# Kernel optimization log

Measured on AMD Instinct MI355X. Metric: run time of the kernel, lower is better.

## Reference

```python
import jax, jax.numpy as jnp
import numpy as np

NEG_INF = jnp.float32(-9e15)
LEAKY_SLOPE = jnp.float32(0.01)  # torch nn.LeakyReLU default


def setup_inputs() -> dict:
    key = jax.random.key(0)
    k1, k2, k3, k4, k5 = jax.random.split(key, 5)
    B, N, din, draw, T = 128, 10000, 64, 64, 8
    D = din + draw
    x = jax.random.normal(k1, (B, N, din), dtype=jnp.float32)
    raw_x = jax.random.normal(k2, (B, N, draw), dtype=jnp.float32)
    # xavier_uniform with gain=1.414 over (D, 1) fan dims
    bound = 1.414 * float(np.sqrt(6.0 / (D + 1)))
    a = jax.random.uniform(k3, (T, D, 1), dtype=jnp.float32, minval=-bound, maxval=bound)
    adj_mask = jax.random.randint(k4, (N,), 0, 2).astype(jnp.float32)
    type_index = jax.random.randint(k5, (B,), 0, T)
    return {"x": x, "raw_x": raw_x, "a": a, "adj_mask": adj_mask,
            "node_index": 0, "type_index": type_index}


def reference(x, raw_x, a, adj_mask, node_index, type_index):
    B, N, _ = x.shape
    T = a.shape[0]
    # broadcast target node features to all nodes and concat with raw features
    target = x[:, node_index, :]                                   # [B, din]
    concat = jnp.concatenate(
        [jnp.broadcast_to(target[:, None, :], (B, N, target.shape[-1])), raw_x],
        axis=-1)                                                   # [B, N, D]
    # per-type additive attention logits (tiny projection D -> 1 per type)
    e = jnp.einsum('bnd,tdo->btn', concat, a)                      # [B, T, N]
    e = jnp.where(e > 0, e, LEAKY_SLOPE * e)                       # LeakyReLU
    masked = jnp.where(adj_mask[None, None, :] > 0, e, NEG_INF)
    att = jax.nn.softmax(masked, axis=-1) * adj_mask[None, None, :]  # [B, T, N]
    # select the attention row matching each sample's type via one-hot
    onehot = jax.nn.one_hot(type_index, T, dtype=att.dtype)        # [B, T]
    probs = jnp.einsum('btn,bt->bn', att, onehot)                  # [B, N]
    return probs
```

## Files before the change

### kernel.cpp

```cpp
#include <hip/hip_runtime.h>
#include <math.h>

#define NEG_INF_F (-9000000000000000.0f)
#define SLOPE 0.01f

constexpr int B_ = 128, N_ = 10000, DIN = 64, DRAW = 64;
constexpr int CHUNK = 1024;
constexpr int NCHUNK = (N_ + CHUNK - 1) / CHUNK;

__global__ __launch_bounds__(256) void pass1_kernel(
    const float* __restrict__ x, const float* __restrict__ raw_x,
    const float* __restrict__ a, const float* __restrict__ adj,
    const int* __restrict__ node_index, const int* __restrict__ type_index,
    float* __restrict__ e_buf, float* __restrict__ pm, float* __restrict__ ps)
{
    const int b = blockIdx.y;
    const int c = blockIdx.x;
    const int tid = threadIdx.x;
    const int t = type_index[b];

    __shared__ float a2[64];
    __shared__ float s_cb;

    if (tid < 64) {
        a2[tid] = a[t * 128 + 64 + tid];
        const int ni = node_index[0];
        float v = x[((size_t)b * N_ + ni) * DIN + tid] * a[t * 128 + tid];
        for (int off = 32; off > 0; off >>= 1) v += __shfl_down(v, off);
        if (tid == 0) s_cb = v;
    }
    __syncthreads();
    const float cb = s_cb;

    float m = NEG_INF_F;
    float s = 0.f;

    const int n0 = c * CHUNK;
    const int n1 = (n0 + CHUNK < N_) ? (n0 + CHUNK) : N_;
    for (int n = n0 + tid; n < n1; n += 256) {
        if (adj[n] > 0.f) {
            const float4* row = (const float4*)(raw_x + ((size_t)b * N_ + n) * DRAW);
            float acc = 0.f;
#pragma unroll
            for (int k = 0; k < 16; ++k) {
                float4 r = row[k];
                acc += r.x * a2[4 * k + 0] + r.y * a2[4 * k + 1]
                     + r.z * a2[4 * k + 2] + r.w * a2[4 * k + 3];
            }
            float e = cb + acc;
            e = (e > 0.f) ? e : SLOPE * e;
            e_buf[(size_t)b * N_ + n] = e;
            if (e > m) { s = s * __expf(m - e) + 1.f; m = e; }
            else       { s += __expf(e - m); }
        }
    }

    __shared__ float sm[256];
    __shared__ float ss[256];
    sm[tid] = m; ss[tid] = s;
    __syncthreads();
    for (int off = 128; off > 0; off >>= 1) {
        if (tid < off) {
            float m2 = sm[tid + off], s2 = ss[tid + off];
            float M = fmaxf(sm[tid], m2);
            ss[tid] = ss[tid] * __expf(sm[tid] - M) + s2 * __expf(m2 - M);
            sm[tid] = M;
        }
        __syncthreads();
    }
    if (tid == 0) {
        pm[b * NCHUNK + c] = sm[0];
        ps[b * NCHUNK + c] = ss[0];
    }
}

__global__ __launch_bounds__(64) void merge_kernel(
    const float* __restrict__ pm, const float* __restrict__ ps,
    float* __restrict__ Mb, float* __restrict__ invSb)
{
    const int b = blockIdx.x;
    const int tid = threadIdx.x;
    float m = NEG_INF_F, s = 0.f;
    if (tid < NCHUNK) { m = pm[b * NCHUNK + tid]; s = ps[b * NCHUNK + tid]; }
    for (int off = 32; off > 0; off >>= 1) {
        float m2 = __shfl_down(m, off);
        float s2 = __shfl_down(s, off);
        float M = fmaxf(m, m2);
        s = s * __expf(m - M) + s2 * __expf(m2 - M);
        m = M;
    }
    if (tid == 0) { Mb[b] = m; invSb[b] = 1.f / s; }
}

__global__ __launch_bounds__(256) void pass3_kernel(
    const float* __restrict__ e_buf, const float* __restrict__ adj,
    const float* __restrict__ Mb, const float* __restrict__ invSb,
    float* __restrict__ out)
{
    const int b = blockIdx.y;
    const int n = blockIdx.x * 256 + threadIdx.x;
    if (n >= N_) return;
    const size_t i = (size_t)b * N_ + n;
    float o = 0.f;
    if (adj[n] > 0.f) o = __expf(e_buf[i] - Mb[b]) * invSb[b];
    out[i] = o;
}

extern "C" void kernel_launch(void* const* d_in, const int* in_sizes, int n_in,
                              void* d_out, int out_size, void* d_ws, size_t ws_size,
                              hipStream_t stream) {
    const float* x     = (const float*)d_in[0];
    const float* raw_x = (const float*)d_in[1];
    const float* a     = (const float*)d_in[2];
    const float* adj   = (const float*)d_in[3];
    const int* node_index = (const int*)d_in[4];
    const int* type_index = (const int*)d_in[5];
    float* out = (float*)d_out;

    float* e_buf = (float*)d_ws;
    float* pm    = e_buf + (size_t)B_ * N_;
    float* ps    = pm + (size_t)B_ * NCHUNK;
    float* Mb    = ps + (size_t)B_ * NCHUNK;
    float* invSb = Mb + B_;

    dim3 g1(NCHUNK, B_);
    pass1_kernel<<<g1, 256, 0, stream>>>(x, raw_x, a, adj, node_index, type_index,
                                         e_buf, pm, ps);
    merge_kernel<<<B_, 64, 0, stream>>>(pm, ps, Mb, invSb);
    dim3 g3((N_ + 255) / 256, B_);
    pass3_kernel<<<g3, 256, 0, stream>>>(e_buf, adj, Mb, invSb, out);
}
```

Baseline: 558.8 us.

## Coalesce raw_x reads with 16-lane row dot products and fold merge into pass3

Pass1 now assigns 16 lanes per row, so each wave reads four contiguous 256-byte rows with float4 loads and reduces them with xor shuffles. Previously each thread walked its own row, which left the raw_x loads strided and uncoalesced. The adjacency chunk is staged in shared memory, and the online softmax state is kept redundantly across the 16 lanes, so the sum is divided by 16. The separate merge kernel is removed: each pass3 block recomputes the per-batch max and sum serially from the chunk partials, and pass3 now uses float4 loads and stores. The cost is redundant exp work per lane, plus partial-merge work repeated in every pass3 block.

Measured after the change: 538.6 us. 1.04x faster.

```diff
diff --git a/kernel.cpp b/kernel.cpp
--- a/kernel.cpp
+++ b/kernel.cpp
@@ -15,15 +15,26 @@
     float* __restrict__ e_buf, float* __restrict__ pm, float* __restrict__ ps)
 {
     const int b = blockIdx.y;
-    const int c = blockIdx.x;
+    const int cblk = blockIdx.x;
     const int tid = threadIdx.x;
+    const int wave = tid >> 6;
+    const int lane = tid & 63;
+    const int r = lane >> 4;
+    const int c = lane & 15;
     const int t = type_index[b];
 
-    __shared__ float a2[64];
+    __shared__ float s_adj[CHUNK];
     __shared__ float s_cb;
 
+    const int n0 = cblk * CHUNK;
+    const int n1 = (n0 + CHUNK < N_) ? (n0 + CHUNK) : N_;
+
+    for (int i = tid; i < CHUNK; i += 256) {
+        const int n = n0 + i;
+        s_adj[i] = (n < N_) ? adj[n] : 0.f;
+    }
+
     if (tid < 64) {
-        a2[tid] = a[t * 128 + 64 + tid];
         const int ni = node_index[0];
         float v = x[((size_t)b * N_ + ni) * DIN + tid] * a[t * 128 + tid];
         for (int off = 32; off > 0; off >>= 1) v += __shfl_down(v, off);
@@ -32,26 +43,26 @@
     __syncthreads();
     const float cb = s_cb;
 
-    float m = NEG_INF_F;
-    float s = 0.f;
+    const float4 a2 = *(const float4*)(a + t * 128 + 64 + c * 4);
 
-    const int n0 = c * CHUNK;
-    const int n1 = (n0 + CHUNK < N_) ? (n0 + CHUNK) : N_;
-    for (int n = n0 + tid; n < n1; n += 256) {
-        if (adj[n] > 0.f) {
-            const float4* row = (const float4*)(raw_x + ((size_t)b * N_ + n) * DRAW);
-            float acc = 0.f;
-#pragma unroll
-            for (int k = 0; k < 16; ++k) {
-                float4 r = row[k];
-                acc += r.x * a2[4 * k + 0] + r.y * a2[4 * k + 1]
-                     + r.z * a2[4 * k + 2] + r.w * a2[4 * k + 3];
-            }
+    float m = NEG_INF_F, s = 0.f;
+
+    for (int base = n0 + wave * 4; base < n1; base += 16) {
+        const int row = base + r;
+        const bool act = s_adj[base - n0 + r] > 0.f;
+        if (act) {
+            const float4 rv = *(const float4*)(raw_x + ((size_t)b * N_ + base) * DRAW + lane * 4);
+            float acc = rv.x * a2.x + rv.y * a2.y + rv.z * a2.z + rv.w * a2.w;
+            acc += __shfl_xor(acc, 1);
+            acc += __shfl_xor(acc, 2);
+            acc += __shfl_xor(acc, 4);
+            acc += __shfl_xor(acc, 8);
             float e = cb + acc;
             e = (e > 0.f) ? e : SLOPE * e;
-            e_buf[(size_t)b * N_ + n] = e;
-            if (e > m) { s = s * __expf(m - e) + 1.f; m = e; }
-            else       { s += __expf(e - m); }
+            const float M = fmaxf(m, e);
+            s = s * __expf(m - M) + __expf(e - M);
+            m = M;
+            if (c == 0) e_buf[(size_t)b * N_ + row] = e;
         }
     }
 
@@ -61,49 +72,51 @@
     __syncthreads();
     for (int off = 128; off > 0; off >>= 1) {
         if (tid < off) {
-            float m2 = sm[tid + off], s2 = ss[tid + off];
-            float M = fmaxf(sm[tid], m2);
+            const float m2 = sm[tid + off], s2 = ss[tid + off];
+            const float M = fmaxf(sm[tid], m2);
             ss[tid] = ss[tid] * __expf(sm[tid] - M) + s2 * __expf(m2 - M);
             sm[tid] = M;
         }
         __syncthreads();
     }
     if (tid == 0) {
-        pm[b * NCHUNK + c] = sm[0];
-        ps[b * NCHUNK + c] = ss[0];
+        pm[b * NCHUNK + cblk] = sm[0];
+        ps[b * NCHUNK + cblk] = ss[0] * (1.f / 16.f);
     }
-}
-
-__global__ __launch_bounds__(64) void merge_kernel(
-    const float* __restrict__ pm, const float* __restrict__ ps,
-    float* __restrict__ Mb, float* __restrict__ invSb)
-{
-    const int b = blockIdx.x;
-    const int tid = threadIdx.x;
-    float m = NEG_INF_F, s = 0.f;
-    if (tid < NCHUNK) { m = pm[b * NCHUNK + tid]; s = ps[b * NCHUNK + tid]; }
-    for (int off = 32; off > 0; off >>= 1) {
-        float m2 = __shfl_down(m, off);
-        float s2 = __shfl_down(s, off);
-        float M = fmaxf(m, m2);
-        s = s * __expf(m - M) + s2 * __expf(m2 - M);
-        m = M;
-    }
-    if (tid == 0) { Mb[b] = m; invSb[b] = 1.f / s; }
 }
 
 __global__ __launch_bounds__(256) void pass3_kernel(
     const float* __restrict__ e_buf, const float* __restrict__ adj,
-    const float* __restrict__ Mb, const float* __restrict__ invSb,
+    const float* __restrict__ pm, const float* __restrict__ ps,
     float* __restrict__ out)
 {
     const int b = blockIdx.y;
-    const int n = blockIdx.x * 256 + threadIdx.x;
-    if (n >= N_) return;
-    const size_t i = (size_t)b * N_ + n;
-    float o = 0.f;
-    if (adj[n] > 0.f) o = __expf(e_buf[i] - Mb[b]) * invSb[b];
-    out[i] = o;
+    const int tid = threadIdx.x;
+
+    __shared__ float sM, sInv;
+    if (tid == 0) {
+        float m = NEG_INF_F, s = 0.f;
+        for (int i = 0; i < NCHUNK; ++i) {
+            const float m2 = pm[b * NCHUNK + i], s2 = ps[b * NCHUNK + i];
+            const float M = fmaxf(m, m2);
+            s = s * __expf(m - M) + s2 * __expf(m2 - M);
+            m = M;
+        }
+        sM = m; sInv = 1.f / s;
+    }
+    __syncthreads();
+    const float M = sM, inv = sInv;
+
+    const int idx4 = blockIdx.x * 256 + tid;
+    if (idx4 >= N_ / 4) return;
+    const float4 a4 = ((const float4*)adj)[idx4];
+    const float4 e4 = ((const float4*)(e_buf + (size_t)b * N_))[idx4];
+    float4 o;
+    o.x = (a4.x > 0.f) ? __expf(e4.x - M) * inv : 0.f;
+    o.y = (a4.y > 0.f) ? __expf(e4.y - M) * inv : 0.f;
+    o.z = (a4.z > 0.f) ? __expf(e4.z - M) * inv : 0.f;
+    o.w = (a4.w > 0.f) ? __expf(e4.w - M) * inv : 0.f;
+    ((float4*)(out + (size_t)b * N_))[idx4] = o;
 }
 
 extern "C" void kernel_launch(void* const* d_in, const int* in_sizes, int n_in,
@@ -120,13 +133,10 @@
     float* e_buf = (float*)d_ws;
     float* pm    = e_buf + (size_t)B_ * N_;
     float* ps    = pm + (size_t)B_ * NCHUNK;
-    float* Mb    = ps + (size_t)B_ * NCHUNK;
-    float* invSb = Mb + B_;
 
     dim3 g1(NCHUNK, B_);
     pass1_kernel<<<g1, 256, 0, stream>>>(x, raw_x, a, adj, node_index, type_index,
                                          e_buf, pm, ps);
-    merge_kernel<<<B_, 64, 0, stream>>>(pm, ps, Mb, invSb);
-    dim3 g3((N_ + 255) / 256, B_);
-    pass3_kernel<<<g3, 256, 0, stream>>>(e_buf, adj, Mb, invSb, out);
+    dim3 g3((N_ / 4 + 255) / 256, B_);
+    pass3_kernel<<<g3, 256, 0, stream>>>(e_buf, adj, pm, ps, out);
 }
```
